# Kernel tuning notes

Measured on AMD Instinct MI355X. Metric: run time of the kernel, lower is better.

## Reference

```python
import jax, jax.numpy as jnp
import numpy as np

B, T, C, H = 8, 2048, 1024, 16
S = C // H
LN_EPS = 1e-5


def setup_inputs() -> dict:
    key = jax.random.key(0)
    ks = jax.random.split(key, 12)
    w = lambda k: jax.random.normal(k, (C, C), dtype=jnp.float32) * 0.02
    return {
        "x": jax.random.normal(ks[0], (B, T, C), dtype=jnp.float32),
        "time_mix_k": jax.random.uniform(ks[1], (1, 1, C), dtype=jnp.float32),
        "time_mix_v": jax.random.uniform(ks[2], (1, 1, C), dtype=jnp.float32),
        "time_mix_r": jax.random.uniform(ks[3], (1, 1, C), dtype=jnp.float32),
        # keep exp(time_decay) < 1 for numerical stability over T=2048 steps
        "time_decay": -jax.random.uniform(ks[4], (H, S), minval=0.1, maxval=5.0, dtype=jnp.float32),
        "time_first": jax.random.uniform(ks[5], (H, S), dtype=jnp.float32),
        "Wk": w(ks[6]), "Wv": w(ks[7]), "Wr": w(ks[8]), "Wo": w(ks[9]),
        "ln_g": jnp.ones((C,), jnp.float32),
        "ln_b": jnp.zeros((C,), jnp.float32),
    }


def reference(x, time_mix_k, time_mix_v, time_mix_r, time_decay, time_first, Wk, Wv, Wr, Wo, ln_g, ln_b):
    Bx, Tx, Cx = x.shape
    # time_shift: xx[t] = x[t-1], xx[0] = 0
    xx = jnp.pad(x, ((0, 0), (1, 0), (0, 0)))[:, :-1]
    xk = x * time_mix_k + xx * (1 - time_mix_k)
    xv = x * time_mix_v + xx * (1 - time_mix_v)
    xr = x * time_mix_r + xx * (1 - time_mix_r)
    proj = lambda z, W: jnp.einsum('btc,dc->btd', z, W).reshape(Bx, Tx, H, S)
    k = proj(xk, Wk)  # [B,T,H,S]
    v = proj(xv, Wv)
    r = proj(xr, Wr)
    kv = k * v  # elementwise per-channel 'at' (diagonal of outer-product state)
    decay = jnp.exp(time_decay)  # [H,S]

    def step(state, inp):
        kv_t, r_t = inp  # [B,H,S] each
        state = kv_t + decay * state
        o = r_t * (time_first * kv_t + state)
        return state, o

    kvT = jnp.swapaxes(kv, 0, 1)  # [T,B,H,S]
    rT = jnp.swapaxes(r, 0, 1)
    _, outT = jax.lax.scan(step, jnp.zeros((Bx, H, S), x.dtype), (kvT, rT))
    out = jnp.swapaxes(outT, 0, 1).reshape(Bx, Tx, Cx)
    mu = out.mean(-1, keepdims=True)
    var = out.var(-1, keepdims=True)
    out = (out - mu) / jnp.sqrt(var + LN_EPS) * ln_g + ln_b
    return jnp.einsum('btc,dc->btd', out, Wo)
```

## Files before the change

### kernel.cpp

```cpp
#include <hip/hip_runtime.h>

#define Bsz 8
#define Tn  2048
#define Cn  1024
#define Hn  16
#define Sn  64
#define Mn  (Bsz * Tn)
#define NC  32
#define LCH (Tn / NC)
#define Kd  1024
#define NKT (Kd / 64)

typedef __attribute__((ext_vector_type(8))) short bf16x8;
typedef __attribute__((ext_vector_type(4))) float f32x4;

__device__ __forceinline__ unsigned short f2bf(float f) {
  union { float f; unsigned int u; } v;
  v.f = f;
  unsigned int r = (v.u + 0x7FFFu + ((v.u >> 16) & 1u)) >> 16;
  return (unsigned short)r;
}
__device__ __forceinline__ float bf2f(unsigned short u) {
  union { unsigned int u; float f; } v;
  v.u = ((unsigned int)u) << 16;
  return v.f;
}

__global__ void wconv_kernel(const float* __restrict__ Wk, const float* __restrict__ Wv,
                             const float* __restrict__ Wr, const float* __restrict__ Wo,
                             unsigned short* __restrict__ out) {
  int i = blockIdx.x * blockDim.x + threadIdx.x;
  int which = i >> 18;
  int off = (i & 0x3FFFF) * 4;
  const float* src = which == 0 ? Wk : which == 1 ? Wv : which == 2 ? Wr : Wo;
  float4 f = *(const float4*)(src + off);
  ushort4 o;
  o.x = f2bf(f.x); o.y = f2bf(f.y); o.z = f2bf(f.z); o.w = f2bf(f.w);
  *(ushort4*)(out + (size_t)which * (Cn * Cn) + off) = o;
}

__global__ void mix3_kernel(const float* __restrict__ x,
                            const float* __restrict__ tmk, const float* __restrict__ tmv,
                            const float* __restrict__ tmr,
                            unsigned short* __restrict__ ok, unsigned short* __restrict__ ov,
                            unsigned short* __restrict__ orr) {
  int idx = blockIdx.x * blockDim.x + threadIdx.x;
  int c4 = idx & (Cn / 4 - 1);
  int bt = idx >> 8;
  int t = bt & (Tn - 1);
  size_t base = (size_t)bt * Cn + c4 * 4;
  float4 xv = *(const float4*)(x + base);
  float4 xxv = {0.f, 0.f, 0.f, 0.f};
  if (t != 0) xxv = *(const float4*)(x + base - Cn);
  float4 dx = {xv.x - xxv.x, xv.y - xxv.y, xv.z - xxv.z, xv.w - xxv.w};
  float4 tk = *(const float4*)(tmk + c4 * 4);
  float4 tv = *(const float4*)(tmv + c4 * 4);
  float4 tr = *(const float4*)(tmr + c4 * 4);
  ushort4 a, b, c;
  a.x = f2bf(xxv.x + tk.x * dx.x); a.y = f2bf(xxv.y + tk.y * dx.y);
  a.z = f2bf(xxv.z + tk.z * dx.z); a.w = f2bf(xxv.w + tk.w * dx.w);
  b.x = f2bf(xxv.x + tv.x * dx.x); b.y = f2bf(xxv.y + tv.y * dx.y);
  b.z = f2bf(xxv.z + tv.z * dx.z); b.w = f2bf(xxv.w + tv.w * dx.w);
  c.x = f2bf(xxv.x + tr.x * dx.x); c.y = f2bf(xxv.y + tr.y * dx.y);
  c.z = f2bf(xxv.z + tr.z * dx.z); c.w = f2bf(xxv.w + tr.w * dx.w);
  *(ushort4*)(ok + base) = a;
  *(ushort4*)(ov + base) = b;
  *(ushort4*)(orr + base) = c;
}

__device__ __forceinline__ void gload_lds16(const void* g, void* l) {
  __builtin_amdgcn_global_load_lds((const __attribute__((address_space(1))) void*)g,
                                   (__attribute__((address_space(3))) void*)l, 16, 0, 0);
}

#define PHASE(H, KS, LOADB, STAGE_STMT, VM_STMT)                                   \
  {                                                                                \
    _Pragma("unroll") for (int mi4 = 0; mi4 < 4; ++mi4) {                          \
      const int row = wm * 128 + (H) * 64 + mi4 * 16 + l15;                        \
      aF[mi4] = *(const bf16x8*)(ldsc + dbase + (KS) * 16384 + row * 64 +          \
                                 ((lg ^ (row & 3)) << 4));                         \
    }                                                                              \
    if (LOADB) {                                                                   \
      _Pragma("unroll") for (int nj = 0; nj < 4; ++nj) {                           \
        const int row = wn * 64 + nj * 16 + l15;                                   \
        bF[nj] = *(const bf16x8*)(ldsc + dbase + 32768 + (KS) * 16384 + row * 64 + \
                                  ((lg ^ (row & 3)) << 4));                        \
      }                                                                            \
    }                                                                              \
    STAGE_STMT;                                                                    \
    VM_STMT;                                                                       \
    __builtin_amdgcn_s_barrier();                                                  \
    asm volatile("s_waitcnt lgkmcnt(0)" ::: "memory");                             \
    __builtin_amdgcn_sched_barrier(0);                                             \
    __builtin_amdgcn_s_setprio(1);                                                 \
    _Pragma("unroll") for (int mi4 = 0; mi4 < 4; ++mi4)                            \
      _Pragma("unroll") for (int nj = 0; nj < 4; ++nj)                             \
        acc[(H) * 4 + mi4][nj] = __builtin_amdgcn_mfma_f32_16x16x32_bf16(          \
            aF[mi4], bF[nj], acc[(H) * 4 + mi4][nj], 0, 0, 0);                     \
    __builtin_amdgcn_s_setprio(0);                                                 \
    __builtin_amdgcn_s_barrier();                                                  \
  }

template <bool OUTBF16>
__global__ __launch_bounds__(512, 2) void gemm8p(const unsigned short* __restrict__ A,
                                                 const unsigned short* __restrict__ Bt,
                                                 void* __restrict__ Cm) {
  __shared__ unsigned short lds[65536];
  char* ldsc = (char*)lds;
  const int tid = threadIdx.x;
  const int wid = tid >> 6, lane = tid & 63;
  const int wm = wid >> 2, wn = wid & 3;
  const int l15 = lane & 15, lg = lane >> 4;
  int bid = ((int)blockIdx.x & 7) * 32 + ((int)blockIdx.x >> 3);
  const int mt = bid >> 2, nt = bid & 3;
  const int m0 = mt * 256, n0 = nt * 256;

  const unsigned short* Ag = A + (size_t)m0 * Kd;
  const unsigned short* Bg = Bt + (size_t)n0 * Kd;

  auto stageR = [&](const unsigned short* gbase, int ktt, int ks, int Loff) {
#pragma unroll
    for (int j = 0; j < 2; ++j) {
      const int row = (tid >> 2) + j * 128;
      const int sl = tid & 3;
      const unsigned short* g =
          gbase + (size_t)row * Kd + ktt * 64 + ks * 32 + ((sl ^ (row & 3)) << 3);
      gload_lds16(g, ldsc + Loff + wid * 1024 + j * 8192);
    }
  };

  f32x4 acc[8][4] = {};
  bf16x8 aF[4], bF[4];

  stageR(Ag, 0, 0, 0);
  stageR(Bg, 0, 0, 32768);
  stageR(Ag, 0, 1, 16384);
  stageR(Bg, 0, 1, 49152);
  stageR(Ag, 1, 0, 65536);
  stageR(Bg, 1, 0, 65536 + 32768);
  asm volatile("s_waitcnt vmcnt(4)" ::: "memory");
  __builtin_amdgcn_s_barrier();

  for (int kt = 0; kt < NKT; ++kt) {
    const int dbase = (kt & 1) << 16;
    const int nd = dbase ^ 65536;
    const bool s1 = (kt + 1 < NKT), s2 = (kt + 2 < NKT);
    const int vmn = (kt < NKT - 2) ? 4 : 0;
    PHASE(0, 0, 1, if (s1) stageR(Ag, kt + 1, 1, nd + 16384), ;)
    PHASE(1, 0, 0, if (s1) stageR(Bg, kt + 1, 1, nd + 49152), ;)
    PHASE(1, 1, 1, if (s2) stageR(Ag, kt + 2, 0, dbase), ;)
    PHASE(0, 1, 0, if (s2) stageR(Bg, kt + 2, 0, dbase + 32768),
          if (vmn == 4) asm volatile("s_waitcnt vmcnt(4)" ::: "memory");
          else asm volatile("s_waitcnt vmcnt(0)" ::: "memory"))
  }

  if (OUTBF16) {
    char* tb = ldsc + wid * 16384;
#pragma unroll
    for (int mi = 0; mi < 8; ++mi)
#pragma unroll
      for (int nj = 0; nj < 4; ++nj)
#pragma unroll
        for (int rr = 0; rr < 4; ++rr) {
          const int row = mi * 16 + lg * 4 + rr;
          const int col = nj * 16 + l15;
          *(unsigned short*)(tb + row * 128 + ((col * 2) ^ ((row & 7) << 4))) =
              f2bf(acc[mi][nj][rr]);
        }
    asm volatile("s_waitcnt lgkmcnt(0)" ::: "memory");
    __builtin_amdgcn_sched_barrier(0);
    const int orl = lane >> 3, och = lane & 7;
#pragma unroll
    for (int it = 0; it < 16; ++it) {
      const int row = it * 8 + orl;
      uint4 vv = *(const uint4*)(tb + row * 128 + ((och * 16) ^ ((row & 7) << 4)));
      const int gr = m0 + wm * 128 + row;
      const int gc = n0 + wn * 64 + och * 8;
      *(uint4*)((unsigned short*)Cm + (size_t)gr * Cn + gc) = vv;
    }
  } else {
#pragma unroll
    for (int mi = 0; mi < 8; ++mi)
#pragma unroll
      for (int nj = 0; nj < 4; ++nj)
#pragma unroll
        for (int rr = 0; rr < 4; ++rr) {
          const int row = m0 + wm * 128 + mi * 16 + lg * 4 + rr;
          const int col = n0 + wn * 64 + nj * 16 + l15;
          ((float*)Cm)[(size_t)row * Cn + col] = acc[mi][nj][rr];
        }
  }
}

__global__ void scan_phase1(const unsigned short* __restrict__ k,
                            const unsigned short* __restrict__ v,
                            const float* __restrict__ td, float* __restrict__ cs) {
  int blk = blockIdx.x;
  int c = blk & (NC - 1);
  int bh = blk >> 5;
  int b = bh >> 4;
  int h = bh & 15;
  int s = threadIdx.x;
  float decay = expf(td[h * Sn + s]);
  size_t base = ((size_t)(b * Tn + c * LCH)) * Cn + h * Sn + s;
  float st = 0.f;
#pragma unroll 8
  for (int i = 0; i < LCH; ++i) {
    float kv = bf2f(k[base]) * bf2f(v[base]);
    st = kv + decay * st;
    base += Cn;
  }
  cs[(size_t)blk * Sn + s] = st;
}

__global__ void scan_phase2(const float* __restrict__ td, float* __restrict__ cs) {
  int bh = blockIdx.x;
  int h = bh & 15;
  int s = threadIdx.x;
  float dL = expf(td[h * Sn + s] * (float)LCH);
  float carry = 0.f;
  for (int c = 0; c < NC; ++c) {
    size_t idx = ((size_t)bh * NC + c) * Sn + s;
    float sc = cs[idx];
    cs[idx] = carry;
    carry = sc + dL * carry;
  }
}

__global__ void scan_phase3(const unsigned short* __restrict__ k,
                            const unsigned short* __restrict__ v,
                            const unsigned short* __restrict__ r,
                            const float* __restrict__ td, const float* __restrict__ tf,
                            const float* __restrict__ cs,
                            unsigned short* __restrict__ out) {
  int blk = blockIdx.x;
  int c = blk & (NC - 1);
  int bh = blk >> 5;
  int b = bh >> 4;
  int h = bh & 15;
  int s = threadIdx.x;
  float decay = expf(td[h * Sn + s]);
  float first = tf[h * Sn + s];
  float st = cs[(size_t)blk * Sn + s];
  size_t base = ((size_t)(b * Tn + c * LCH)) * Cn + h * Sn + s;
#pragma unroll 8
  for (int i = 0; i < LCH; ++i) {
    float kv = bf2f(k[base]) * bf2f(v[base]);
    st = kv + decay * st;
    out[base] = f2bf(bf2f(r[base]) * (first * kv + st));
    base += Cn;
  }
}

__global__ __launch_bounds__(256) void ln_kernel(const unsigned short* __restrict__ in,
                                                 const float* __restrict__ g,
                                                 const float* __restrict__ bb,
                                                 unsigned short* __restrict__ out) {
  int row = blockIdx.x;
  int tid = threadIdx.x;
  size_t base = (size_t)row * Cn + tid * 4;
  ushort4 uv = *(const ushort4*)(in + base);
  float4 xv = {bf2f(uv.x), bf2f(uv.y), bf2f(uv.z), bf2f(uv.w)};
  float sum = xv.x + xv.y + xv.z + xv.w;
  float ss = xv.x * xv.x + xv.y * xv.y + xv.z * xv.z + xv.w * xv.w;
#pragma unroll
  for (int off = 32; off >= 1; off >>= 1) {
    sum += __shfl_down(sum, off, 64);
    ss += __shfl_down(ss, off, 64);
  }
  __shared__ float s1[4], s2[4];
  if ((tid & 63) == 0) { s1[tid >> 6] = sum; s2[tid >> 6] = ss; }
  __syncthreads();
  sum = s1[0] + s1[1] + s1[2] + s1[3];
  ss = s2[0] + s2[1] + s2[2] + s2[3];
  float mu = sum * (1.f / Cn);
  float var = ss * (1.f / Cn) - mu * mu;
  float rstd = rsqrtf(var + 1e-5f);
  float4 gv = *(const float4*)(g + tid * 4);
  float4 bv = *(const float4*)(bb + tid * 4);
  ushort4 o;
  o.x = f2bf((xv.x - mu) * rstd * gv.x + bv.x);
  o.y = f2bf((xv.y - mu) * rstd * gv.y + bv.y);
  o.z = f2bf((xv.z - mu) * rstd * gv.z + bv.z);
  o.w = f2bf((xv.w - mu) * rstd * gv.w + bv.w);
  *(ushort4*)(out + base) = o;
}

extern "C" void kernel_launch(void* const* d_in, const int* in_sizes, int n_in,
                              void* d_out, int out_size, void* d_ws, size_t ws_size,
                              hipStream_t stream) {
  const float* x   = (const float*)d_in[0];
  const float* tmk = (const float*)d_in[1];
  const float* tmv = (const float*)d_in[2];
  const float* tmr = (const float*)d_in[3];
  const float* td  = (const float*)d_in[4];
  const float* tf  = (const float*)d_in[5];
  const float* Wk  = (const float*)d_in[6];
  const float* Wv  = (const float*)d_in[7];
  const float* Wr  = (const float*)d_in[8];
  const float* Wo  = (const float*)d_in[9];
  const float* lng = (const float*)d_in[10];
  const float* lnb = (const float*)d_in[11];
  float* out = (float*)d_out;

  char* ws = (char*)d_ws;
  const size_t MB = 1024 * 1024;
  unsigned short* wbf  = (unsigned short*)(ws);
  unsigned short* xk   = (unsigned short*)(ws + 8 * MB);
  unsigned short* xv_  = (unsigned short*)(ws + 40 * MB);
  unsigned short* xr   = (unsigned short*)(ws + 72 * MB);
  unsigned short* bufK = (unsigned short*)(ws + 104 * MB);
  unsigned short* bufV = (unsigned short*)(ws + 136 * MB);
  unsigned short* bufR = (unsigned short*)(ws + 168 * MB);
  unsigned short* preLN = xk;
  unsigned short* lnout = xv_;
  float* chunkS = (float*)(ws + 200 * MB);

  const int gemm_grid = (Mn / 256) * (Cn / 256);
  const int mix_grid = Mn * (Cn / 4) / 256;

  wconv_kernel<<<4 * Cn * Cn / 4 / 256, 256, 0, stream>>>(Wk, Wv, Wr, Wo, wbf);
  mix3_kernel<<<mix_grid, 256, 0, stream>>>(x, tmk, tmv, tmr, xk, xv_, xr);

  gemm8p<true><<<gemm_grid, 512, 0, stream>>>(xk,  wbf + 0 * (size_t)Cn * Cn, bufK);
  gemm8p<true><<<gemm_grid, 512, 0, stream>>>(xv_, wbf + 1 * (size_t)Cn * Cn, bufV);
  gemm8p<true><<<gemm_grid, 512, 0, stream>>>(xr,  wbf + 2 * (size_t)Cn * Cn, bufR);

  scan_phase1<<<Bsz * Hn * NC, 64, 0, stream>>>(bufK, bufV, td, chunkS);
  scan_phase2<<<Bsz * Hn, 64, 0, stream>>>(td, chunkS);
  scan_phase3<<<Bsz * Hn * NC, 64, 0, stream>>>(bufK, bufV, bufR, td, tf, chunkS, preLN);

  ln_kernel<<<Mn, 256, 0, stream>>>(preLN, lng, lnb, lnout);

  gemm8p<false><<<gemm_grid, 512, 0, stream>>>(lnout, wbf + 3 * (size_t)Cn * Cn, out);

  (void)in_sizes; (void)n_in; (void)out_size; (void)ws_size;
}
```

Before: 257.6 us.

## Stage full K-tile per phase with 128-byte rows and 8-way XOR swizzle

Changes the GEMM LDS layout from two 64-byte half-K slabs per tile to full 128-byte rows with an 8-way XOR swizzle. It replaces the staggered prefetch schedule, which loaded the next halves across four phases with a two-deep lookahead, with a single full next-tile load at the first phase and a vmcnt(0) wait at the last phase. The aim is simpler, more contiguous global-to-LDS copies and fewer bank conflicts. In exchange, prefetch depth drops to one tile and all loads are issued in one burst, which may expose more memory latency.

```diff
diff --git a/kernel.cpp b/kernel.cpp
--- a/kernel.cpp
+++ b/kernel.cpp
@@ -73,22 +73,21 @@
                                    (__attribute__((address_space(3))) void*)l, 16, 0, 0);
 }
 
-#define PHASE(H, KS, LOADB, STAGE_STMT, VM_STMT)                                   \
+#define PHASE(H, KS, LOADB, PRE)                                                   \
   {                                                                                \
     _Pragma("unroll") for (int mi4 = 0; mi4 < 4; ++mi4) {                          \
       const int row = wm * 128 + (H) * 64 + mi4 * 16 + l15;                        \
-      aF[mi4] = *(const bf16x8*)(ldsc + dbase + (KS) * 16384 + row * 64 +          \
-                                 ((lg ^ (row & 3)) << 4));                         \
+      aF[mi4] = *(const bf16x8*)(ldsc + dbase + row * 128 +                        \
+                                 ((((KS) * 4 + lg) ^ (row & 7)) << 4));            \
     }                                                                              \
     if (LOADB) {                                                                   \
       _Pragma("unroll") for (int nj = 0; nj < 4; ++nj) {                           \
         const int row = wn * 64 + nj * 16 + l15;                                   \
-        bF[nj] = *(const bf16x8*)(ldsc + dbase + 32768 + (KS) * 16384 + row * 64 + \
-                                  ((lg ^ (row & 3)) << 4));                        \
+        bF[nj] = *(const bf16x8*)(ldsc + dbase + 32768 + row * 128 +               \
+                                  ((((KS) * 4 + lg) ^ (row & 7)) << 4));           \
       }                                                                            \
     }                                                                              \
-    STAGE_STMT;                                                                    \
-    VM_STMT;                                                                       \
+    PRE;                                                                           \
     __builtin_amdgcn_s_barrier();                                                  \
     asm volatile("s_waitcnt lgkmcnt(0)" ::: "memory");                             \
     __builtin_amdgcn_sched_barrier(0);                                             \
@@ -118,40 +117,37 @@
   const unsigned short* Ag = A + (size_t)m0 * Kd;
   const unsigned short* Bg = Bt + (size_t)n0 * Kd;
 
-  auto stageR = [&](const unsigned short* gbase, int ktt, int ks, int Loff) {
+  auto stageU = [&](const unsigned short* gbase, int ktt, int rbase, int Loff) {
 #pragma unroll
     for (int j = 0; j < 2; ++j) {
-      const int row = (tid >> 2) + j * 128;
-      const int sl = tid & 3;
-      const unsigned short* g =
-          gbase + (size_t)row * Kd + ktt * 64 + ks * 32 + ((sl ^ (row & 3)) << 3);
-      gload_lds16(g, ldsc + Loff + wid * 1024 + j * 8192);
+      const int il = j * 512 + tid;
+      const int r = rbase + (il >> 3);
+      const int c = (il & 7) ^ (r & 7);
+      gload_lds16(gbase + (size_t)r * Kd + ktt * 64 + c * 8,
+                  ldsc + Loff + rbase * 128 + il * 16);
     }
   };
+  auto stageKT = [&](int ktt, int base) {
+    stageU(Ag, ktt, 0, base);
+    stageU(Ag, ktt, 128, base);
+    stageU(Bg, ktt, 0, base + 32768);
+    stageU(Bg, ktt, 128, base + 32768);
+  };
 
   f32x4 acc[8][4] = {};
   bf16x8 aF[4], bF[4];
 
-  stageR(Ag, 0, 0, 0);
-  stageR(Bg, 0, 0, 32768);
-  stageR(Ag, 0, 1, 16384);
-  stageR(Bg, 0, 1, 49152);
-  stageR(Ag, 1, 0, 65536);
-  stageR(Bg, 1, 0, 65536 + 32768);
-  asm volatile("s_waitcnt vmcnt(4)" ::: "memory");
+  stageKT(0, 0);
+  asm volatile("s_waitcnt vmcnt(0)" ::: "memory");
   __builtin_amdgcn_s_barrier();
 
   for (int kt = 0; kt < NKT; ++kt) {
     const int dbase = (kt & 1) << 16;
     const int nd = dbase ^ 65536;
-    const bool s1 = (kt + 1 < NKT), s2 = (kt + 2 < NKT);
-    const int vmn = (kt < NKT - 2) ? 4 : 0;
-    PHASE(0, 0, 1, if (s1) stageR(Ag, kt + 1, 1, nd + 16384), ;)
-    PHASE(1, 0, 0, if (s1) stageR(Bg, kt + 1, 1, nd + 49152), ;)
-    PHASE(1, 1, 1, if (s2) stageR(Ag, kt + 2, 0, dbase), ;)
-    PHASE(0, 1, 0, if (s2) stageR(Bg, kt + 2, 0, dbase + 32768),
-          if (vmn == 4) asm volatile("s_waitcnt vmcnt(4)" ::: "memory");
-          else asm volatile("s_waitcnt vmcnt(0)" ::: "memory"))
+    PHASE(0, 0, 1, if (kt + 1 < NKT) stageKT(kt + 1, nd))
+    PHASE(1, 0, 0, ;)
+    PHASE(1, 1, 1, ;)
+    PHASE(0, 1, 0, asm volatile("s_waitcnt vmcnt(0)" ::: "memory"))
   }
 
   if (OUTBF16) {
```

Measured after the change: 255.1 us. No clear change (-0.9%).
